# Optimization experiments

Measured on AMD Instinct MI355X. Metric: run time of the kernel, lower is better.

## Reference

```python
import jax, jax.numpy as jnp
import numpy as np

TEMPERATURE = 0.1
EPS = 1e-8  # torch F.cosine_similarity norm clamp


def setup_inputs() -> dict:
    key = jax.random.key(0)
    k1, k2, k3 = jax.random.split(key, 3)
    N, E = 4096, 256
    return {
        "tab_unique": jax.random.normal(k1, (N, E), jnp.float32),
        "ts_anchor": jax.random.normal(k2, (N, E), jnp.float32),
        "labels": jax.random.randint(k3, (N,), 0, 100),
    }


def reference(tab_unique, ts_anchor, labels):
    N = tab_unique.shape[0]
    # Stack views, normalize once, single GEMM for cosine similarity (2N,2N)
    z = jnp.concatenate([tab_unique, ts_anchor], axis=0)
    zn = z / jnp.maximum(jnp.linalg.norm(z, axis=1, keepdims=True), EPS)
    sim = zn @ zn.T  # (2N, 2N)

    dl = jnp.concatenate([labels, labels], axis=0)  # (2N,)
    mask = (dl[:, None] == dl[None, :]).astype(sim.dtype)  # (2N, 2N)

    masked_sim = sim * mask
    # cross-view blocks: top-right and bottom-left (N, N) each
    positives = jnp.concatenate([masked_sim[:N, N:], masked_sim[N:, :N]], axis=0)  # (2N, N)

    # denominator: exp(sim/T) with self-similarity zeroed, row sum
    not_self = ~jnp.eye(2 * N, dtype=bool)
    denom = jnp.sum(jnp.where(not_self, jnp.exp(sim / TEMPERATURE), 0.0), axis=1, keepdims=True)  # (2N, 1)

    logits = positives / TEMPERATURE - jnp.log(denom)  # (2N, N)
    grouped = jnp.sum(logits, axis=1) / jnp.sum(mask, axis=1)  # (2N,)
    return -jnp.sum(grouped) / (2 * N)
```

## Files before the change

kernel.cpp:

```cpp
#include <hip/hip_runtime.h>
#include <hip/hip_bf16.h>
#include <math.h>

typedef __bf16 bf16x8 __attribute__((ext_vector_type(8)));
typedef __bf16 bf16x4 __attribute__((ext_vector_type(4)));
typedef float  f32x4  __attribute__((ext_vector_type(4)));

#define N_ROWS 4096
#define E_DIM  256
#define TWO_N  (2 * N_ROWS)
#define BT 128
#define BK 64
#define NSLOT 65
#define SQRT_L 3.798282567081813f

__device__ __forceinline__ void gload_lds16(const void* g, void* l) {
    __builtin_amdgcn_global_load_lds(
        (const __attribute__((address_space(1))) void*)g,
        (__attribute__((address_space(3))) void*)l,
        16, 0, 0);
}

__global__ __launch_bounds__(256) void prep_kernel(
    const float* __restrict__ tab, const float* __restrict__ ts,
    __hip_bfloat16* __restrict__ zn)
{
    const int tid  = threadIdx.x;
    const int wave = tid >> 6, lane = tid & 63;
    const int row  = blockIdx.x * 4 + wave;

    const float* src = row < N_ROWS ? tab + (size_t)row * E_DIM
                                    : ts + (size_t)(row - N_ROWS) * E_DIM;
    const float4 v = *(const float4*)(src + lane * 4);
    float ss = v.x * v.x + v.y * v.y + v.z * v.z + v.w * v.w;
    #pragma unroll
    for (int m = 32; m >= 1; m >>= 1) ss += __shfl_xor(ss, m);
    const float inv = SQRT_L / fmaxf(sqrtf(ss), 1e-8f);
    bf16x4 o = { (__bf16)(v.x * inv), (__bf16)(v.y * inv),
                 (__bf16)(v.z * inv), (__bf16)(v.w * inv) };
    *(bf16x4*)(zn + (size_t)row * E_DIM + lane * 4) = o;
}

__global__ __launch_bounds__(256, 4) void simloss_kernel(
    const __hip_bfloat16* __restrict__ zn,
    const int* __restrict__ labels,
    float* __restrict__ rowExpP,
    float* __restrict__ rowPosP)
{
    const int i = blockIdx.x;
    const int d = blockIdx.y;
    if (d == 32 && i >= 32) return;
    const int j = (i + d) & 63;

    const int rb = i * BT;
    const int cb = j * BT;

    __shared__ __align__(16) char ldsS[32768];
    __shared__ int labRow[BT];
    __shared__ int labCol[BT];

    char* ldsA = ldsS;
    char* ldsB = ldsS + 16384;

    const int tid  = threadIdx.x;
    const int lane = tid & 63;
    const int wave = tid >> 6;
    const int wr = wave >> 1, wc = wave & 1;
    const int l15 = lane & 15, lg = lane >> 4;

    if (tid < BT)      labRow[tid]      = labels[(rb + tid) & (N_ROWS - 1)];
    else               labCol[tid - BT] = labels[(cb + tid - BT) & (N_ROWS - 1)];

    f32x4 acc[4][4];
    #pragma unroll
    for (int a = 0; a < 4; ++a)
        #pragma unroll
        for (int b = 0; b < 4; ++b) acc[a][b] = (f32x4){0.f, 0.f, 0.f, 0.f};

    #pragma unroll
    for (int kt = 0; kt < E_DIM / BK; ++kt) {
        #pragma unroll
        for (int it = 0; it < 4; ++it) {
            const int idx = it * 256 + wave * 64 + lane;
            const int row = idx >> 3;
            const int sch = (idx & 7) ^ (row & 7);
            gload_lds16(zn + (size_t)(rb + row) * E_DIM + kt * BK + sch * 8,
                        ldsA + (it * 256 + wave * 64) * 16);
            gload_lds16(zn + (size_t)(cb + row) * E_DIM + kt * BK + sch * 8,
                        ldsB + (it * 256 + wave * 64) * 16);
        }
        __syncthreads();

        #pragma unroll
        for (int ks = 0; ks < 2; ++ks) {
            bf16x8 af[4], bfr[4];
            #pragma unroll
            for (int rf = 0; rf < 4; ++rf) {
                const int r = wr * 64 + rf * 16 + l15;
                af[rf] = *(const bf16x8*)(ldsA + r * 128 + (((ks * 4 + lg) ^ (r & 7)) << 4));
            }
            #pragma unroll
            for (int cf = 0; cf < 4; ++cf) {
                const int c = wc * 64 + cf * 16 + l15;
                bfr[cf] = *(const bf16x8*)(ldsB + c * 128 + (((ks * 4 + lg) ^ (c & 7)) << 4));
            }
            #pragma unroll
            for (int rf = 0; rf < 4; ++rf)
                #pragma unroll
                for (int cf = 0; cf < 4; ++cf)
                    acc[rf][cf] = __builtin_amdgcn_mfma_f32_16x16x32_bf16(af[rf], bfr[cf], acc[rf][cf], 0, 0, 0);
        }
        __syncthreads();
    }

    const bool isDiag = (d == 0);
    const bool cross  = (i < 32) != (j < 32);

    float* tblRow = (float*)ldsS;
    float* tblCol = (float*)(ldsS + 22528);

    int cl[4], clab[4];
    #pragma unroll
    for (int cf = 0; cf < 4; ++cf) {
        cl[cf]   = wc * 64 + cf * 16 + l15;
        clab[cf] = labCol[cl[cf]];
    }

    float colE[4] = {0.f, 0.f, 0.f, 0.f};
    float colP[4] = {0.f, 0.f, 0.f, 0.f};

    #pragma unroll
    for (int rf = 0; rf < 4; ++rf) {
        #pragma unroll
        for (int jj = 0; jj < 4; ++jj) {
            const int rloc = wr * 64 + rf * 16 + lg * 4 + jj;
            const int rlab = labRow[rloc];
            float rowE = 0.f;
            #pragma unroll
            for (int cf = 0; cf < 4; ++cf) {
                const float s = acc[rf][cf][jj];
                float e = __builtin_amdgcn_exp2f(s);
                if (isDiag && rloc == cl[cf]) e = 0.f;
                rowE += e;
                colE[cf] += e;
                if (cross && rlab == clab[cf]) colP[cf] += s;
            }
            tblRow[rloc * 44 + wc * 16 + l15] = rowE;
        }
    }
    #pragma unroll
    for (int cf = 0; cf < 4; ++cf)
        tblCol[cl[cf] * 12 + wr * 4 + lg] = colE[cf];

    __syncthreads();

    if (tid < 128) {
        const float* rp = tblRow + tid * 44;
        const int rot = (tid >> 3) & 7;
        float es = 0.f;
        #pragma unroll
        for (int c0 = 0; c0 < 8; ++c0) {
            const int ch = (c0 + rot) & 7;
            f32x4 v = *(const f32x4*)(rp + ch * 4);
            es += v[0] + v[1] + v[2] + v[3];
        }
        rowExpP[(size_t)d * TWO_N + rb + tid] = es;

        if (d > 0) {
            const float* cp = tblCol + tid * 12;
            f32x4 a = *(const f32x4*)(cp);
            f32x4 b = *(const f32x4*)(cp + 4);
            const float ec = a[0]+a[1]+a[2]+a[3] + b[0]+b[1]+b[2]+b[3];
            rowExpP[(size_t)(32 + d) * TWO_N + cb + tid] = ec;
        }
    }

    if (cross) {
        __syncthreads();
        #pragma unroll
        for (int rf = 0; rf < 4; ++rf) {
            #pragma unroll
            for (int jj = 0; jj < 4; ++jj) {
                const int rloc = wr * 64 + rf * 16 + lg * 4 + jj;
                const int rlab = labRow[rloc];
                float rowP = 0.f;
                #pragma unroll
                for (int cf = 0; cf < 4; ++cf)
                    if (rlab == clab[cf]) rowP += acc[rf][cf][jj];
                tblRow[rloc * 44 + wc * 16 + l15] = rowP;
            }
        }
        #pragma unroll
        for (int cf = 0; cf < 4; ++cf)
            tblCol[cl[cf] * 12 + wr * 4 + lg] = colP[cf];
        __syncthreads();
        if (tid < 128) {
            const float* rp = tblRow + tid * 44;
            const int rot = (tid >> 3) & 7;
            float ps = 0.f;
            #pragma unroll
            for (int c0 = 0; c0 < 8; ++c0) {
                const int ch = (c0 + rot) & 7;
                f32x4 v = *(const f32x4*)(rp + ch * 4);
                ps += v[0] + v[1] + v[2] + v[3];
            }
            rowPosP[(size_t)d * TWO_N + rb + tid] = ps;
            if (d > 0) {
                const float* cp = tblCol + tid * 12;
                f32x4 a = *(const f32x4*)(cp);
                f32x4 b = *(const f32x4*)(cp + 4);
                rowPosP[(size_t)(32 + d) * TWO_N + cb + tid] =
                    a[0]+a[1]+a[2]+a[3] + b[0]+b[1]+b[2]+b[3];
            }
        }
    } else {
        if (tid < 128) {
            rowPosP[(size_t)d * TWO_N + rb + tid] = 0.f;
            if (d > 0) rowPosP[(size_t)(32 + d) * TWO_N + cb + tid] = 0.f;
        }
    }

    if (d == 32 && tid < 128) {
        rowExpP[(size_t)64 * TWO_N + rb + tid] = 0.f;
        rowExpP[(size_t)32 * TWO_N + cb + tid] = 0.f;
        rowPosP[(size_t)64 * TWO_N + rb + tid] = 0.f;
        rowPosP[(size_t)32 * TWO_N + cb + tid] = 0.f;
    }
}

__global__ __launch_bounds__(256) void fin1_kernel(
    const float* __restrict__ rowExpP, const float* __restrict__ rowPosP,
    const int* __restrict__ labels, double* __restrict__ partial)
{
    __shared__ int hist[128];
    const int tid = threadIdx.x;
    if (tid < 128) hist[tid] = 0;
    __syncthreads();
    for (int idx = tid; idx < N_ROWS; idx += 256) atomicAdd(&hist[labels[idx]], 1);
    __syncthreads();

    const int r = blockIdx.x * 256 + tid;
    float es = 0.f;
    #pragma unroll 5
    for (int s = 0; s < NSLOT; ++s) es += rowExpP[(size_t)s * TWO_N + r];
    float ps = 0.f;
    #pragma unroll 5
    for (int s = 0; s < NSLOT; ++s) ps += rowPosP[(size_t)s * TWO_N + r];

    const int lab = labels[r & (N_ROWS - 1)];
    double g = ((double)ps * 0.6931471805599453 - (double)N_ROWS * log((double)es))
               / (2.0 * (double)hist[lab]);

    #pragma unroll
    for (int m = 32; m >= 1; m >>= 1) g += __shfl_xor(g, m);
    __shared__ double wsum[4];
    const int wave = tid >> 6, lane = tid & 63;
    if (lane == 0) wsum[wave] = g;
    __syncthreads();
    if (tid == 0) partial[blockIdx.x] = wsum[0] + wsum[1] + wsum[2] + wsum[3];
}

__global__ void fin2_kernel(const double* __restrict__ partial, float* __restrict__ out) {
    if (threadIdx.x == 0) {
        double tot = 0.0;
        for (int b = 0; b < 32; ++b) tot += partial[b];
        out[0] = (float)(-tot / (double)TWO_N);
    }
}

extern "C" void kernel_launch(void* const* d_in, const int* in_sizes, int n_in,
                              void* d_out, int out_size, void* d_ws, size_t ws_size,
                              hipStream_t stream) {
    const float* tab    = (const float*)d_in[0];
    const float* ts     = (const float*)d_in[1];
    const int*   labels = (const int*)d_in[2];

    char* ws = (char*)d_ws;
    __hip_bfloat16* zn = (__hip_bfloat16*)ws;
    const size_t znBytes = (size_t)TWO_N * E_DIM * sizeof(__hip_bfloat16);
    float* rowExpP = (float*)(ws + znBytes);
    float* rowPosP = rowExpP + (size_t)NSLOT * TWO_N;
    double* partial = (double*)(rowPosP + (size_t)NSLOT * TWO_N);

    prep_kernel<<<TWO_N / 4, 256, 0, stream>>>(tab, ts, zn);

    dim3 grid(64, 33);
    simloss_kernel<<<grid, 256, 0, stream>>>(zn, labels, rowExpP, rowPosP);

    fin1_kernel<<<32, 256, 0, stream>>>(rowExpP, rowPosP, labels, partial);
    fin2_kernel<<<1, 64, 0, stream>>>(partial, (float*)d_out);
}
```

Measured before the change: 57.69 us.

## Fuse final reduction kernels into simloss via atomic counter and spin-wait blocks

Removes the two finalization kernel launches by reusing the 32 idle blocks in the last grid row of the similarity kernel. Those blocks spin on a global counter until all 2080 producer tiles have signalled, then do the per-row reduction. A second counter picks the last block, which writes the scalar output. This removes launch gaps but relies on the idle blocks not starving producers of CU slots, and adds atomics and fences.

```diff
diff --git a/kernel.cpp b/kernel.cpp
--- a/kernel.cpp
+++ b/kernel.cpp
@@ -12,6 +12,7 @@
 #define BT 128
 #define BK 64
 #define NSLOT 65
+#define NPROD 2080
 #define SQRT_L 3.798282567081813f
 
 __device__ __forceinline__ void gload_lds16(const void* g, void* l) {
@@ -23,11 +24,13 @@
 
 __global__ __launch_bounds__(256) void prep_kernel(
     const float* __restrict__ tab, const float* __restrict__ ts,
-    __hip_bfloat16* __restrict__ zn)
+    __hip_bfloat16* __restrict__ zn, int* __restrict__ cnt)
 {
     const int tid  = threadIdx.x;
     const int wave = tid >> 6, lane = tid & 63;
     const int row  = blockIdx.x * 4 + wave;
+
+    if (blockIdx.x == 0 && tid < 2) cnt[tid] = 0;
 
     const float* src = row < N_ROWS ? tab + (size_t)row * E_DIM
                                     : ts + (size_t)(row - N_ROWS) * E_DIM;
@@ -45,24 +48,74 @@
     const __hip_bfloat16* __restrict__ zn,
     const int* __restrict__ labels,
     float* __restrict__ rowExpP,
-    float* __restrict__ rowPosP)
+    float* __restrict__ rowPosP,
+    double* __restrict__ partial,
+    int* __restrict__ cnt,
+    float* __restrict__ out)
 {
     const int i = blockIdx.x;
     const int d = blockIdx.y;
-    if (d == 32 && i >= 32) return;
-    const int j = (i + d) & 63;
-
-    const int rb = i * BT;
-    const int cb = j * BT;
 
     __shared__ __align__(16) char ldsS[32768];
     __shared__ int labRow[BT];
     __shared__ int labCol[BT];
 
+    const int tid  = threadIdx.x;
+
+    if (d == 32 && i >= 32) {
+        if (tid == 0) {
+            while (__hip_atomic_load(&cnt[0], __ATOMIC_ACQUIRE,
+                                     __HIP_MEMORY_SCOPE_AGENT) < NPROD)
+                __builtin_amdgcn_s_sleep(8);
+        }
+        __syncthreads();
+
+        int* hist = (int*)ldsS;
+        double* wsum = (double*)(ldsS + 1024);
+        if (tid < 128) hist[tid] = 0;
+        __syncthreads();
+        for (int idx = tid; idx < N_ROWS; idx += 256) atomicAdd(&hist[labels[idx]], 1);
+        __syncthreads();
+
+        const int slice = i - 32;
+        const int r = slice * 256 + tid;
+        float es = 0.f;
+        #pragma unroll 5
+        for (int s = 0; s < NSLOT; ++s) es += rowExpP[(size_t)s * TWO_N + r];
+        float ps = 0.f;
+        #pragma unroll 5
+        for (int s = 0; s < NSLOT; ++s) ps += rowPosP[(size_t)s * TWO_N + r];
+
+        const int lab = labels[r & (N_ROWS - 1)];
+        double g = ((double)ps * 0.6931471805599453 - (double)N_ROWS * log((double)es))
+                   / (2.0 * (double)hist[lab]);
+
+        #pragma unroll
+        for (int m = 32; m >= 1; m >>= 1) g += __shfl_xor(g, m);
+        const int wave = tid >> 6, lane = tid & 63;
+        if (lane == 0) wsum[wave] = g;
+        __syncthreads();
+        if (tid == 0) {
+            partial[slice] = wsum[0] + wsum[1] + wsum[2] + wsum[3];
+            __threadfence();
+            const int t2 = atomicAdd(&cnt[1], 1);
+            if (t2 == 31) {
+                __threadfence();
+                double tot = 0.0;
+                for (int b = 0; b < 32; ++b) tot += partial[b];
+                out[0] = (float)(-tot / (double)TWO_N);
+            }
+        }
+        return;
+    }
+
+    const int j = (i + d) & 63;
+    const int rb = i * BT;
+    const int cb = j * BT;
+
     char* ldsA = ldsS;
     char* ldsB = ldsS + 16384;
 
-    const int tid  = threadIdx.x;
     const int lane = tid & 63;
     const int wave = tid >> 6;
     const int wr = wave >> 1, wc = wave & 1;
@@ -170,8 +223,8 @@
             const float* cp = tblCol + tid * 12;
             f32x4 a = *(const f32x4*)(cp);
             f32x4 b = *(const f32x4*)(cp + 4);
-            const float ec = a[0]+a[1]+a[2]+a[3] + b[0]+b[1]+b[2]+b[3];
-            rowExpP[(size_t)(32 + d) * TWO_N + cb + tid] = ec;
+            rowExpP[(size_t)(32 + d) * TWO_N + cb + tid] =
+                a[0]+a[1]+a[2]+a[3] + b[0]+b[1]+b[2]+b[3];
         }
     }
 
@@ -226,45 +279,11 @@
         rowPosP[(size_t)64 * TWO_N + rb + tid] = 0.f;
         rowPosP[(size_t)32 * TWO_N + cb + tid] = 0.f;
     }
-}
-
-__global__ __launch_bounds__(256) void fin1_kernel(
-    const float* __restrict__ rowExpP, const float* __restrict__ rowPosP,
-    const int* __restrict__ labels, double* __restrict__ partial)
-{
-    __shared__ int hist[128];
-    const int tid = threadIdx.x;
-    if (tid < 128) hist[tid] = 0;
+
     __syncthreads();
-    for (int idx = tid; idx < N_ROWS; idx += 256) atomicAdd(&hist[labels[idx]], 1);
-    __syncthreads();
-
-    const int r = blockIdx.x * 256 + tid;
-    float es = 0.f;
-    #pragma unroll 5
-    for (int s = 0; s < NSLOT; ++s) es += rowExpP[(size_t)s * TWO_N + r];
-    float ps = 0.f;
-    #pragma unroll 5
-    for (int s = 0; s < NSLOT; ++s) ps += rowPosP[(size_t)s * TWO_N + r];
-
-    const int lab = labels[r & (N_ROWS - 1)];
-    double g = ((double)ps * 0.6931471805599453 - (double)N_ROWS * log((double)es))
-               / (2.0 * (double)hist[lab]);
-
-    #pragma unroll
-    for (int m = 32; m >= 1; m >>= 1) g += __shfl_xor(g, m);
-    __shared__ double wsum[4];
-    const int wave = tid >> 6, lane = tid & 63;
-    if (lane == 0) wsum[wave] = g;
-    __syncthreads();
-    if (tid == 0) partial[blockIdx.x] = wsum[0] + wsum[1] + wsum[2] + wsum[3];
-}
-
-__global__ void fin2_kernel(const double* __restrict__ partial, float* __restrict__ out) {
-    if (threadIdx.x == 0) {
-        double tot = 0.0;
-        for (int b = 0; b < 32; ++b) tot += partial[b];
-        out[0] = (float)(-tot / (double)TWO_N);
+    if (tid == 0) {
+        __threadfence();
+        atomicAdd(&cnt[0], 1);
     }
 }
 
@@ -281,12 +300,11 @@
     float* rowExpP = (float*)(ws + znBytes);
     float* rowPosP = rowExpP + (size_t)NSLOT * TWO_N;
     double* partial = (double*)(rowPosP + (size_t)NSLOT * TWO_N);
-
-    prep_kernel<<<TWO_N / 4, 256, 0, stream>>>(tab, ts, zn);
+    int* cnt = (int*)(partial + 32);
+
+    prep_kernel<<<TWO_N / 4, 256, 0, stream>>>(tab, ts, zn, cnt);
 
     dim3 grid(64, 33);
-    simloss_kernel<<<grid, 256, 0, stream>>>(zn, labels, rowExpP, rowPosP);
-
-    fin1_kernel<<<32, 256, 0, stream>>>(rowExpP, rowPosP, labels, partial);
-    fin2_kernel<<<1, 64, 0, stream>>>(partial, (float*)d_out);
+    simloss_kernel<<<grid, 256, 0, stream>>>(zn, labels, rowExpP, rowPosP,
+                                             partial, cnt, (float*)d_out);
 }
```

Measured after the change: 127.3 us. 121% more time.
